# Kernel optimization log

Measured on AMD Instinct MI355X. Metric: run time of the kernel, lower is better.

## Reference

```python
import jax, jax.numpy as jnp
import numpy as np

NEG = -1e30
H = 768

def mask_logits(target, mask):
    return target * mask + (1.0 - mask) * NEG

def setup_inputs() -> dict:
    key = jax.random.key(0)
    ks = jax.random.split(key, 8)
    B, CL, QL = 16, 512, 64
    c = jax.random.normal(ks[0], (B, CL, H), dtype=jnp.float32)
    q = jax.random.normal(ks[1], (B, QL, H), dtype=jnp.float32)
    c_mask = jnp.ones((B, CL), dtype=jnp.float32)
    q_mask = jnp.ones((B, QL), dtype=jnp.float32)
    # nn.Linear(768,1) weights (kaiming-ish scale) and biases
    std = 1.0 / np.sqrt(H)
    w_c = jax.random.normal(ks[2], (H,), dtype=jnp.float32) * std
    w_q = jax.random.normal(ks[3], (H,), dtype=jnp.float32) * std
    w_cq = jax.random.normal(ks[4], (H,), dtype=jnp.float32) * std
    b_c = jax.random.normal(ks[5], (), dtype=jnp.float32) * std
    b_q = jax.random.normal(ks[6], (), dtype=jnp.float32) * std
    b_cq = jax.random.normal(ks[7], (), dtype=jnp.float32) * std
    return {"c": c, "q": q, "c_mask": c_mask, "q_mask": q_mask,
            "w_c": w_c, "b_c": b_c, "w_q": w_q, "b_q": b_q,
            "w_cq": w_cq, "b_cq": b_cq}

def reference(c, q, c_mask, q_mask, w_c, b_c, w_q, b_q, w_cq, b_cq):
    # c: (B, c_len, H), q: (B, q_len, H)
    cm = c_mask[:, :, None]   # (B, c_len, 1)
    qm = q_mask[:, None, :]   # (B, 1, q_len)
    # per-query loop in torch == trilinear term: ((c*w_cq) @ q^T) + b_cq
    cq = jnp.einsum('bid,bjd->bij', c * w_cq, q) + b_cq      # (B, c_len, q_len)
    s = (c @ w_c + b_c)[:, :, None] + (q @ w_q + b_q)[:, None, :] + cq
    a = jax.nn.softmax(mask_logits(s, qm), axis=2)            # (B, c_len, q_len)
    c2q = jnp.einsum('bij,bjd->bid', a, q)                    # (B, c_len, H)
    b_att = jax.nn.softmax(jnp.max(mask_logits(s, cm), axis=2), axis=1)  # (B, c_len)
    q2c = jnp.einsum('bi,bid->bd', b_att, c)[:, None, :]      # (B, 1, H)
    x = jnp.concatenate([c, c2q, c * c2q, c * q2c], axis=-1)  # (B, c_len, 4H)
    return x
```

## Files before the change

kernel.cpp:

```cpp
#include <hip/hip_runtime.h>
#include <math.h>
#include <stdint.h>

#define NEGV -1e30f
typedef unsigned short u16;
typedef unsigned int u32;
typedef short bfx8 __attribute__((ext_vector_type(8)));
typedef float f32x4 __attribute__((ext_vector_type(4)));

constexpr int B_  = 16;
constexpr int CL  = 512;
constexpr int QL  = 64;
constexpr int H   = 768;
constexpr int OD  = 4 * H;
constexpr int IT  = 16;
constexpr int OSTR = 772;

constexpr size_t WS_QW     = 0;
constexpr size_t WS_ROWMAX = 1024;
constexpr size_t WS_PART   = 17408;
constexpr size_t WS_QBF    = 422912;
constexpr size_t WS_QTF    = 816128;

__device__ __forceinline__ u16 f2b(float x) {
  u32 u = __float_as_uint(x);
  u += 0x7FFFu + ((u >> 16) & 1u);
  return (u16)(u >> 16);
}
__device__ __forceinline__ float wredmax(float v) {
#pragma unroll
  for (int off = 32; off; off >>= 1) v = fmaxf(v, __shfl_xor(v, off));
  return v;
}
__device__ __forceinline__ float wredsum(float v) {
#pragma unroll
  for (int off = 32; off; off >>= 1) v += __shfl_xor(v, off);
  return v;
}

__global__ __launch_bounds__(256) void k_qprep(const float* __restrict__ q,
                                               const float* __restrict__ w_cq,
                                               const float* __restrict__ w_q,
                                               const float* __restrict__ b_q,
                                               const float* __restrict__ b_cq,
                                               u16* __restrict__ qbF,
                                               u16* __restrict__ qTF,
                                               float* __restrict__ qw) {
  const int ch = blockIdx.x, bb = blockIdx.y, t = threadIdx.x;
  if (ch == 6) {
    int j = t >> 2, qt = t & 3;
    const float* qr = q + ((size_t)bb * QL + j) * H;
    float s = 0.f;
#pragma unroll 8
    for (int p = 0; p < 48; ++p) {
      float4 v = *(const float4*)(qr + (qt * 48 + p) * 4);
      float4 w = *(const float4*)(w_q + (qt * 48 + p) * 4);
      s += v.x * w.x + v.y * w.y + v.z * w.z + v.w * w.w;
    }
    s += __shfl_xor(s, 1);
    s += __shfl_xor(s, 2);
    if (qt == 0) qw[bb * QL + j] = s + b_q[0] + b_cq[0];
    return;
  }
  __shared__ u16 tR[64 * 132], tS[64 * 132];
  const int d0 = ch * 128;
#pragma unroll
  for (int s2 = 0; s2 < 8; ++s2) {
    int idx = t + s2 * 256, j = idx >> 5, d4 = idx & 31;
    size_t go = ((size_t)(bb * QL + j)) * H + d0 + d4 * 4;
    float4 v = *(const float4*)(q + go);
    float4 w = *(const float4*)(w_cq + d0 + d4 * 4);
    uint2 raw, scl;
    raw.x = f2b(v.x) | ((u32)f2b(v.y) << 16);
    raw.y = f2b(v.z) | ((u32)f2b(v.w) << 16);
    scl.x = f2b(v.x * w.x) | ((u32)f2b(v.y * w.y) << 16);
    scl.y = f2b(v.z * w.z) | ((u32)f2b(v.w * w.w) << 16);
    *(uint2*)&tR[j * 132 + d4 * 4] = raw;
    *(uint2*)&tS[j * 132 + d4 * 4] = scl;
  }
  __syncthreads();
  {
    int l = t & 63, jt = t >> 6, lr = l & 15, lg = l >> 4;
#pragma unroll
    for (int kt = 0; kt < 4; ++kt) {
      u16 vals[8];
#pragma unroll
      for (int e = 0; e < 8; ++e)
        vals[e] = tS[(jt * 16 + lr) * 132 + kt * 32 + lg * 8 + e];
      uint4 pk;
      pk.x = vals[0] | ((u32)vals[1] << 16);
      pk.y = vals[2] | ((u32)vals[3] << 16);
      pk.z = vals[4] | ((u32)vals[5] << 16);
      pk.w = vals[6] | ((u32)vals[7] << 16);
      *(uint4*)(qbF + ((((size_t)bb * 4 + jt) * 24) + ch * 4 + kt) * 512 + l * 8) = pk;
    }
  }
  {
#pragma unroll
    for (int rep = 0; rep < 4; ++rep) {
      int idx = rep * 256 + t;
      int l = idx & 63, h = (idx >> 6) & 1, uul = idx >> 7;
      int lr = l & 15, lg = l >> 4;
      u16 vals[8];
#pragma unroll
      for (int e = 0; e < 8; ++e)
        vals[e] = tR[(h * 32 + lg * 8 + e) * 132 + uul * 16 + lr];
      uint4 pk;
      pk.x = vals[0] | ((u32)vals[1] << 16);
      pk.y = vals[2] | ((u32)vals[3] << 16);
      pk.z = vals[4] | ((u32)vals[5] << 16);
      pk.w = vals[6] | ((u32)vals[7] << 16);
      *(uint4*)(qTF + (((size_t)bb * 48 + ch * 8 + uul) * 2 + h) * 512 + l * 8) = pk;
    }
  }
}

__global__ __launch_bounds__(256, 2) void ka(const float* __restrict__ c,
                                             const float* __restrict__ c_mask,
                                             const float* __restrict__ q_mask,
                                             const float* __restrict__ w_c,
                                             const float* __restrict__ b_c,
                                             const float* __restrict__ qw,
                                             const u16* __restrict__ qbF,
                                             const u16* __restrict__ qTF,
                                             float* __restrict__ rowmax,
                                             float* __restrict__ out) {
  __shared__ __align__(16) char shm[IT * OSTR * 4];
  __shared__ float sS[IT * 68];
  __shared__ u16 aS[IT * 64];
  float* oS = (float*)shm;

  const int t = threadIdx.x, lane = t & 63;
  const int wid = __builtin_amdgcn_readfirstlane(t >> 6);
  const int bb = blockIdx.y, i0 = blockIdx.x * IT;
  const int lr = lane & 15, lg = lane >> 4;
  const int sw = (lr & 7) << 4;

  const u16* qbp = qbF + (((size_t)bb * 4 + wid) * 24) * 512 + lane * 8;
  const u16* qtp = qTF + (size_t)bb * 49152 + lane * 8;

  bfx8 qpf0 = *(const bfx8*)(qbp);
  bfx8 qpf1 = *(const bfx8*)(qbp + 512);

  float cwq = 0.f;
  {
    int row = t >> 4, c4b = t & 15;
    size_t cb0 = ((size_t)bb * CL + i0 + row) * H;
#pragma unroll
    for (int u = 0; u < 12; ++u) {
      int col4 = c4b + u * 16;
      float4 v = *(const float4*)(c + cb0 + col4 * 4);
      float4 w = *(const float4*)(w_c + col4 * 4);
      cwq += v.x * w.x + v.y * w.y + v.z * w.z + v.w * w.w;
      uint2 pk;
      pk.x = f2b(v.x) | ((u32)f2b(v.y) << 16);
      pk.y = f2b(v.z) | ((u32)f2b(v.w) << 16);
      int byte = row * 1536 + ((col4 * 8) ^ ((row & 7) << 4));
      *(uint2*)(shm + byte) = pk;
    }
    cwq += __shfl_xor(cwq, 1);
    cwq += __shfl_xor(cwq, 2);
    cwq += __shfl_xor(cwq, 4);
    cwq += __shfl_xor(cwq, 8);
  }
  const float qw_r = qw[bb * QL + lane];
  const float qm_r = q_mask[bb * QL + lane];
  const float bc = b_c[0];
  __syncthreads();

  f32x4 acc0 = {0.f, 0.f, 0.f, 0.f}, acc1 = {0.f, 0.f, 0.f, 0.f};
  {
    const char* ap = shm + lr * 1536;
    acc0 = __builtin_amdgcn_mfma_f32_16x16x32_bf16(
        *(const bfx8*)(ap + ((lg * 16) ^ sw)), qpf0, acc0, 0, 0, 0);
    acc1 = __builtin_amdgcn_mfma_f32_16x16x32_bf16(
        *(const bfx8*)(ap + ((64 + lg * 16) ^ sw)), qpf1, acc1, 0, 0, 0);
#pragma unroll
    for (int kt = 2; kt < 24; kt += 2) {
      bfx8 av0 = *(const bfx8*)(ap + ((kt * 64 + lg * 16) ^ sw));
      bfx8 av1 = *(const bfx8*)(ap + (((kt + 1) * 64 + lg * 16) ^ sw));
      bfx8 bv0 = *(const bfx8*)(qbp + kt * 512);
      bfx8 bv1 = *(const bfx8*)(qbp + (kt + 1) * 512);
      acc0 = __builtin_amdgcn_mfma_f32_16x16x32_bf16(av0, bv0, acc0, 0, 0, 0);
      acc1 = __builtin_amdgcn_mfma_f32_16x16x32_bf16(av1, bv1, acc1, 0, 0, 0);
    }
  }
  bfx8 pf0 = *(const bfx8*)(qtp + (size_t)(wid * 12 + 0) * 1024);
  bfx8 pf1 = *(const bfx8*)(qtp + (size_t)(wid * 12 + 0) * 1024 + 512);
  bfx8 pf2 = *(const bfx8*)(qtp + (size_t)(wid * 12 + 1) * 1024);
  bfx8 pf3 = *(const bfx8*)(qtp + (size_t)(wid * 12 + 1) * 1024 + 512);
#pragma unroll
  for (int m = 0; m < 4; ++m)
    sS[(lg * 4 + m) * 68 + wid * 16 + lr] = acc0[m] + acc1[m];
  __syncthreads();

#pragma unroll
  for (int rr = 0; rr < 4; ++rr) {
    int r = wid * 4 + rr;
    float s = sS[r * 68 + lane] + qw_r;
    float mraw = wredmax(s);
    float sm = (qm_r > 0.5f) ? s : NEGV;
    float mm = wredmax(sm);
    float p = __expf(sm - mm);
    float ps = wredsum(p);
    float a = p / ps;
    float cwr = __shfl(cwq, rr * 16);
    if (lane == 0) {
      float cmv = c_mask[bb * CL + i0 + r];
      rowmax[bb * CL + i0 + r] = (cmv > 0.5f) ? (mraw + cwr + bc) : NEGV;
    }
    int byte = r * 128 + ((lane * 2) ^ ((r & 7) << 4));
    *(u16*)((char*)aS + byte) = f2b(a);
  }
  __syncthreads();

  bfx8 a0 = *(const bfx8*)((char*)aS + lr * 128 + ((lg * 16) ^ sw));
  bfx8 a1 = *(const bfx8*)((char*)aS + lr * 128 + ((64 + lg * 16) ^ sw));
  f32x4 o[12];
  {
    f32x4 v0 = {0.f, 0.f, 0.f, 0.f};
    v0 = __builtin_amdgcn_mfma_f32_16x16x32_bf16(a0, pf0, v0, 0, 0, 0);
    v0 = __builtin_amdgcn_mfma_f32_16x16x32_bf16(a1, pf1, v0, 0, 0, 0);
    o[0] = v0;
    f32x4 v1 = {0.f, 0.f, 0.f, 0.f};
    v1 = __builtin_amdgcn_mfma_f32_16x16x32_bf16(a0, pf2, v1, 0, 0, 0);
    v1 = __builtin_amdgcn_mfma_f32_16x16x32_bf16(a1, pf3, v1, 0, 0, 0);
    o[1] = v1;
  }
#pragma unroll
  for (int u = 2; u < 12; ++u) {
    int uu = wid * 12 + u;
    bfx8 b0 = *(const bfx8*)(qtp + (size_t)uu * 1024);
    bfx8 b1 = *(const bfx8*)(qtp + (size_t)uu * 1024 + 512);
    f32x4 v = {0.f, 0.f, 0.f, 0.f};
    v = __builtin_amdgcn_mfma_f32_16x16x32_bf16(a0, b0, v, 0, 0, 0);
    v = __builtin_amdgcn_mfma_f32_16x16x32_bf16(a1, b1, v, 0, 0, 0);
    o[u] = v;
  }

#pragma unroll
  for (int u = 0; u < 12; ++u) {
    int d = wid * 192 + u * 16 + lr;
#pragma unroll
    for (int m = 0; m < 4; ++m)
      oS[(lg * 4 + m) * OSTR + d] = o[u][m];
  }
  __syncthreads();
  {
    int row = t >> 4, c4b = t & 15;
    size_t grow = (size_t)bb * CL + i0 + row;
    const float* crow = c + grow * H;
    float* ob = out + grow * OD;
#pragma unroll
    for (int k = 0; k < 12; ++k) {
      int d = (c4b + k * 16) * 4;
      float4 cv = *(const float4*)(crow + d);
      float4 ov = *(const float4*)&oS[row * OSTR + d];
      *(float4*)(ob + d) = cv;
      *(float4*)(ob + H + d) = ov;
      *(float4*)(ob + 2 * H + d) = make_float4(cv.x * ov.x, cv.y * ov.y,
                                               cv.z * ov.z, cv.w * ov.w);
    }
  }
}

__global__ __launch_bounds__(256) void kb(const float* __restrict__ rowmax,
                                          const float* __restrict__ c,
                                          float* __restrict__ part) {
  int s = blockIdx.x, b = blockIdx.y, t = threadIdx.x;
  __shared__ float red[8];
  __shared__ float ba[16];
  float v0 = rowmax[b * CL + t], v1 = rowmax[b * CL + t + 256];
  float m = wredmax(fmaxf(v0, v1));
  if ((t & 63) == 0) red[t >> 6] = m;
  __syncthreads();
  m = fmaxf(fmaxf(red[0], red[1]), fmaxf(red[2], red[3]));
  float p = __expf(v0 - m) + __expf(v1 - m);
  p = wredsum(p);
  if ((t & 63) == 0) red[4 + (t >> 6)] = p;
  __syncthreads();
  float ssum = red[4] + red[5] + red[6] + red[7];
  if (t < 16) ba[t] = __expf(rowmax[b * CL + s * 16 + t] - m) / ssum;
  __syncthreads();
  if (t < 192) {
    const float* cb = c + ((size_t)b * CL + s * 16) * H;
    float4 acc = make_float4(0.f, 0.f, 0.f, 0.f);
#pragma unroll
    for (int r = 0; r < 16; ++r) {
      float w = ba[r];
      float4 cv = *(const float4*)(cb + (size_t)r * H + t * 4);
      acc.x += w * cv.x; acc.y += w * cv.y; acc.z += w * cv.z; acc.w += w * cv.w;
    }
    *(float4*)(part + ((size_t)b * 32 + s) * H + t * 4) = acc;
  }
}

__global__ __launch_bounds__(256) void kc2(const float* __restrict__ part,
                                           const float* __restrict__ c,
                                           float* __restrict__ out) {
  __shared__ float4 redS[8][32];
  __shared__ float4 q2cS[32];
  const int b = blockIdx.y;
  const int s = blockIdx.x >> 4, rg = blockIdx.x & 15;
  const int t = threadIdx.x;
  const int grp = t >> 5, col4 = t & 31;
  float4 acc = make_float4(0.f, 0.f, 0.f, 0.f);
#pragma unroll
  for (int u = 0; u < 4; ++u) {
    float4 v = *(const float4*)(part + ((size_t)b * 32 + grp * 4 + u) * H +
                                s * 128 + col4 * 4);
    acc.x += v.x; acc.y += v.y; acc.z += v.z; acc.w += v.w;
  }
  redS[grp][col4] = acc;
  __syncthreads();
  if (t < 32) {
    float4 sum = redS[0][t];
#pragma unroll
    for (int g = 1; g < 8; ++g) {
      float4 v = redS[g][t];
      sum.x += v.x; sum.y += v.y; sum.z += v.z; sum.w += v.w;
    }
    q2cS[t] = sum;
  }
  __syncthreads();
  float4 gv = q2cS[col4];
  const int sub = t >> 5;
#pragma unroll
  for (int r2 = 0; r2 < 4; ++r2) {
    int row = rg * 32 + sub * 4 + r2;
    size_t grow = (size_t)b * CL + row;
    float4 cv = *(const float4*)(c + grow * H + s * 128 + col4 * 4);
    *(float4*)(out + grow * OD + 3 * H + s * 128 + col4 * 4) =
        make_float4(cv.x * gv.x, cv.y * gv.y, cv.z * gv.z, cv.w * gv.w);
  }
}

extern "C" void kernel_launch(void* const* d_in, const int* in_sizes, int n_in,
                              void* d_out, int out_size, void* d_ws, size_t ws_size,
                              hipStream_t stream) {
  const float* c      = (const float*)d_in[0];
  const float* q      = (const float*)d_in[1];
  const float* c_mask = (const float*)d_in[2];
  const float* q_mask = (const float*)d_in[3];
  const float* w_c    = (const float*)d_in[4];
  const float* b_c    = (const float*)d_in[5];
  const float* w_q    = (const float*)d_in[6];
  const float* b_q    = (const float*)d_in[7];
  const float* w_cq   = (const float*)d_in[8];
  const float* b_cq   = (const float*)d_in[9];
  float* out = (float*)d_out;
  float* ws  = (float*)d_ws;
  float* qw     = ws + WS_QW;
  float* rowmax = ws + WS_ROWMAX;
  float* part   = ws + WS_PART;
  u16*   qbF    = (u16*)(ws + WS_QBF);
  u16*   qTF    = (u16*)(ws + WS_QTF);

  k_qprep<<<dim3(7, B_), 256, 0, stream>>>(q, w_cq, w_q, b_q, b_cq, qbF, qTF, qw);
  ka<<<dim3(CL / IT, B_), 256, 0, stream>>>(c, c_mask, q_mask, w_c, b_c,
                                            qw, qbF, qTF, rowmax, out);
  kb<<<dim3(32, B_), 256, 0, stream>>>(rowmax, c, part);
  kc2<<<dim3(96, B_), 256, 0, stream>>>(part, c, out);
}
```

Measured before the change: 58.26 us.

## Swap MFMA operands to write c2q directly from registers, drop LDS staging

The c2q MFMA operands are swapped so each lane holds four consecutive output columns of one row. The output is then written straight from registers as float4, removing the LDS transpose buffer and a block barrier. The smaller shared footprint allows a launch bound of 4 blocks per CU. The q2c partial kernel now handles 32 rows per block with half as many blocks, and the reduction reads fewer partials. Risks: the global write pattern is now 16 rows times 64 bytes per wave, which may coalesce worse than full-row stores.

After: 58.38 us (median of 2 runs). Within noise of the previous version (+0.2%).

```diff
diff --git a/kernel.cpp b/kernel.cpp
--- a/kernel.cpp
+++ b/kernel.cpp
@@ -14,7 +14,6 @@
 constexpr int H   = 768;
 constexpr int OD  = 4 * H;
 constexpr int IT  = 16;
-constexpr int OSTR = 772;
 
 constexpr size_t WS_QW     = 0;
 constexpr size_t WS_ROWMAX = 1024;
@@ -115,7 +114,7 @@
   }
 }
 
-__global__ __launch_bounds__(256, 2) void ka(const float* __restrict__ c,
+__global__ __launch_bounds__(256, 4) void ka(const float* __restrict__ c,
                                              const float* __restrict__ c_mask,
                                              const float* __restrict__ q_mask,
                                              const float* __restrict__ w_c,
@@ -125,10 +124,9 @@
                                              const u16* __restrict__ qTF,
                                              float* __restrict__ rowmax,
                                              float* __restrict__ out) {
-  __shared__ __align__(16) char shm[IT * OSTR * 4];
+  __shared__ __align__(16) u16 cA[IT * H];
   __shared__ float sS[IT * 68];
   __shared__ u16 aS[IT * 64];
-  float* oS = (float*)shm;
 
   const int t = threadIdx.x, lane = t & 63;
   const int wid = __builtin_amdgcn_readfirstlane(t >> 6);
@@ -156,7 +154,7 @@
       pk.x = f2b(v.x) | ((u32)f2b(v.y) << 16);
       pk.y = f2b(v.z) | ((u32)f2b(v.w) << 16);
       int byte = row * 1536 + ((col4 * 8) ^ ((row & 7) << 4));
-      *(uint2*)(shm + byte) = pk;
+      *(uint2*)((char*)cA + byte) = pk;
     }
     cwq += __shfl_xor(cwq, 1);
     cwq += __shfl_xor(cwq, 2);
@@ -170,7 +168,7 @@
 
   f32x4 acc0 = {0.f, 0.f, 0.f, 0.f}, acc1 = {0.f, 0.f, 0.f, 0.f};
   {
-    const char* ap = shm + lr * 1536;
+    const char* ap = (const char*)cA + lr * 1536;
     acc0 = __builtin_amdgcn_mfma_f32_16x16x32_bf16(
         *(const bfx8*)(ap + ((lg * 16) ^ sw)), qpf0, acc0, 0, 0, 0);
     acc1 = __builtin_amdgcn_mfma_f32_16x16x32_bf16(
@@ -219,12 +217,12 @@
   f32x4 o[12];
   {
     f32x4 v0 = {0.f, 0.f, 0.f, 0.f};
-    v0 = __builtin_amdgcn_mfma_f32_16x16x32_bf16(a0, pf0, v0, 0, 0, 0);
-    v0 = __builtin_amdgcn_mfma_f32_16x16x32_bf16(a1, pf1, v0, 0, 0, 0);
+    v0 = __builtin_amdgcn_mfma_f32_16x16x32_bf16(pf0, a0, v0, 0, 0, 0);
+    v0 = __builtin_amdgcn_mfma_f32_16x16x32_bf16(pf1, a1, v0, 0, 0, 0);
     o[0] = v0;
     f32x4 v1 = {0.f, 0.f, 0.f, 0.f};
-    v1 = __builtin_amdgcn_mfma_f32_16x16x32_bf16(a0, pf2, v1, 0, 0, 0);
-    v1 = __builtin_amdgcn_mfma_f32_16x16x32_bf16(a1, pf3, v1, 0, 0, 0);
+    v1 = __builtin_amdgcn_mfma_f32_16x16x32_bf16(pf2, a0, v1, 0, 0, 0);
+    v1 = __builtin_amdgcn_mfma_f32_16x16x32_bf16(pf3, a1, v1, 0, 0, 0);
     o[1] = v1;
   }
 #pragma unroll
@@ -233,33 +231,24 @@
     bfx8 b0 = *(const bfx8*)(qtp + (size_t)uu * 1024);
     bfx8 b1 = *(const bfx8*)(qtp + (size_t)uu * 1024 + 512);
     f32x4 v = {0.f, 0.f, 0.f, 0.f};
-    v = __builtin_amdgcn_mfma_f32_16x16x32_bf16(a0, b0, v, 0, 0, 0);
-    v = __builtin_amdgcn_mfma_f32_16x16x32_bf16(a1, b1, v, 0, 0, 0);
+    v = __builtin_amdgcn_mfma_f32_16x16x32_bf16(b0, a0, v, 0, 0, 0);
+    v = __builtin_amdgcn_mfma_f32_16x16x32_bf16(b1, a1, v, 0, 0, 0);
     o[u] = v;
   }
 
-#pragma unroll
-  for (int u = 0; u < 12; ++u) {
-    int d = wid * 192 + u * 16 + lr;
-#pragma unroll
-    for (int m = 0; m < 4; ++m)
-      oS[(lg * 4 + m) * OSTR + d] = o[u][m];
-  }
-  __syncthreads();
-  {
-    int row = t >> 4, c4b = t & 15;
-    size_t grow = (size_t)bb * CL + i0 + row;
+  {
+    size_t grow = (size_t)bb * CL + i0 + lr;
     const float* crow = c + grow * H;
     float* ob = out + grow * OD;
 #pragma unroll
-    for (int k = 0; k < 12; ++k) {
-      int d = (c4b + k * 16) * 4;
-      float4 cv = *(const float4*)(crow + d);
-      float4 ov = *(const float4*)&oS[row * OSTR + d];
-      *(float4*)(ob + d) = cv;
-      *(float4*)(ob + H + d) = ov;
-      *(float4*)(ob + 2 * H + d) = make_float4(cv.x * ov.x, cv.y * ov.y,
-                                               cv.z * ov.z, cv.w * ov.w);
+    for (int u = 0; u < 12; ++u) {
+      int d4 = (wid * 12 + u) * 16 + lg * 4;
+      float4 cv = *(const float4*)(crow + d4);
+      float4 ov = make_float4(o[u][0], o[u][1], o[u][2], o[u][3]);
+      *(float4*)(ob + d4) = cv;
+      *(float4*)(ob + H + d4) = ov;
+      *(float4*)(ob + 2 * H + d4) = make_float4(cv.x * ov.x, cv.y * ov.y,
+                                                cv.z * ov.z, cv.w * ov.w);
     }
   }
 }
@@ -269,7 +258,7 @@
                                           float* __restrict__ part) {
   int s = blockIdx.x, b = blockIdx.y, t = threadIdx.x;
   __shared__ float red[8];
-  __shared__ float ba[16];
+  __shared__ float ba[32];
   float v0 = rowmax[b * CL + t], v1 = rowmax[b * CL + t + 256];
   float m = wredmax(fmaxf(v0, v1));
   if ((t & 63) == 0) red[t >> 6] = m;
@@ -280,18 +269,18 @@
   if ((t & 63) == 0) red[4 + (t >> 6)] = p;
   __syncthreads();
   float ssum = red[4] + red[5] + red[6] + red[7];
-  if (t < 16) ba[t] = __expf(rowmax[b * CL + s * 16 + t] - m) / ssum;
+  if (t < 32) ba[t] = __expf(rowmax[b * CL + s * 32 + t] - m) / ssum;
   __syncthreads();
   if (t < 192) {
-    const float* cb = c + ((size_t)b * CL + s * 16) * H;
+    const float* cb = c + ((size_t)b * CL + s * 32) * H;
     float4 acc = make_float4(0.f, 0.f, 0.f, 0.f);
-#pragma unroll
-    for (int r = 0; r < 16; ++r) {
+#pragma unroll 8
+    for (int r = 0; r < 32; ++r) {
       float w = ba[r];
       float4 cv = *(const float4*)(cb + (size_t)r * H + t * 4);
       acc.x += w * cv.x; acc.y += w * cv.y; acc.z += w * cv.z; acc.w += w * cv.w;
     }
-    *(float4*)(part + ((size_t)b * 32 + s) * H + t * 4) = acc;
+    *(float4*)(part + ((size_t)b * 16 + s) * H + t * 4) = acc;
   }
 }
 
@@ -306,8 +295,8 @@
   const int grp = t >> 5, col4 = t & 31;
   float4 acc = make_float4(0.f, 0.f, 0.f, 0.f);
 #pragma unroll
-  for (int u = 0; u < 4; ++u) {
-    float4 v = *(const float4*)(part + ((size_t)b * 32 + grp * 4 + u) * H +
+  for (int u = 0; u < 2; ++u) {
+    float4 v = *(const float4*)(part + ((size_t)b * 16 + grp * 2 + u) * H +
                                 s * 128 + col4 * 4);
     acc.x += v.x; acc.y += v.y; acc.z += v.z; acc.w += v.w;
   }
@@ -359,6 +348,6 @@
   k_qprep<<<dim3(7, B_), 256, 0, stream>>>(q, w_cq, w_q, b_q, b_cq, qbF, qTF, qw);
   ka<<<dim3(CL / IT, B_), 256, 0, stream>>>(c, c_mask, q_mask, w_c, b_c,
                                             qw, qbF, qTF, rowmax, out);
-  kb<<<dim3(32, B_), 256, 0, stream>>>(rowmax, c, part);
+  kb<<<dim3(16, B_), 256, 0, stream>>>(rowmax, c, part);
   kc2<<<dim3(96, B_), 256, 0, stream>>>(part, c, out);
 }
```
